# Kernel optimization log

Hardware: AMD Instinct MI355X
Metric: run time of the kernel (lower is better)

## Reference

```python
import jax, jax.numpy as jnp
import numpy as np

HIDDEN = 2048
N_HEADS = 16
N_KV = 4
HEAD_DIM = 128
B, T = 2, 2048


def setup_inputs() -> dict:
    key = jax.random.key(0)
    k1, k2, k3, k4 = jax.random.split(key, 4)
    x = jax.random.normal(k1, (B, T, HIDDEN), dtype=jnp.float32)
    # linear weights stored [out, in] like torch; we apply x @ W.T
    w_q = jax.random.normal(k2, (N_HEADS * HEAD_DIM, HIDDEN), dtype=jnp.float32) * (HIDDEN ** -0.5)
    w_kv = jax.random.normal(k3, (2 * N_KV * HEAD_DIM, HIDDEN), dtype=jnp.float32) * (HIDDEN ** -0.5)
    w_o = jax.random.normal(k4, (HIDDEN, N_HEADS * HEAD_DIM), dtype=jnp.float32) * ((N_HEADS * HEAD_DIM) ** -0.5)
    return {"x": x, "w_q": w_q, "w_kv": w_kv, "w_o": w_o}


def reference(x, w_q, w_kv, w_o):
    b, t, _ = x.shape
    groups = N_HEADS // N_KV
    scale = HEAD_DIM ** -0.5

    q = (x @ w_q.T).reshape(b, t, N_HEADS, HEAD_DIM).transpose(0, 2, 1, 3)  # [B,H,T,D]
    kv = x @ w_kv.T
    k, v = jnp.split(kv, 2, axis=-1)
    k = k.reshape(b, t, N_KV, HEAD_DIM).transpose(0, 2, 1, 3)  # [B,KV,T,D]
    v = v.reshape(b, t, N_KV, HEAD_DIM).transpose(0, 2, 1, 3)
    # repeat_interleave over head dim -> [B,H,T,D]
    k = jnp.repeat(k, groups, axis=1)
    v = jnp.repeat(v, groups, axis=1)

    scores = jnp.einsum('bhqd,bhkd->bhqk', q, k) * scale  # [B,H,T,T]
    causal = jnp.triu(jnp.ones((t, t), dtype=bool), k=1)
    scores = jnp.where(causal, -jnp.inf, scores)
    weights = jax.nn.softmax(scores, axis=-1)
    out = jnp.einsum('bhqk,bhkd->bhqd', weights, v)  # [B,H,T,D]
    out = out.transpose(0, 2, 1, 3).reshape(b, t, N_HEADS * HEAD_DIM)
    return out @ w_o.T
```

## Files before the change

### kernel.cpp

```cpp
#include <hip/hip_runtime.h>

typedef short bf16x8 __attribute__((ext_vector_type(8)));
typedef float f32x4 __attribute__((ext_vector_type(4)));
typedef unsigned int u32x4 __attribute__((ext_vector_type(4)));

__device__ __forceinline__ unsigned short f2bf(float f) {
    unsigned int u = __float_as_uint(f);
    u = (u + 0x7fff + ((u >> 16) & 1)) >> 16;
    return (unsigned short)u;
}
__device__ __forceinline__ float bf2f(short s) {
    return __uint_as_float(((unsigned int)(unsigned short)s) << 16);
}

__device__ __forceinline__ void async16(const void* g, void* l) {
    __builtin_amdgcn_global_load_lds(
        (const __attribute__((address_space(1))) void*)g,
        (__attribute__((address_space(3))) void*)l,
        16 , 0 , 0 );
}

__global__ __launch_bounds__(256) void castall(const float* __restrict__ x,
                                               const float* __restrict__ wq,
                                               const float* __restrict__ wkv,
                                               const float* __restrict__ wo,
                                               unsigned short* __restrict__ xb,
                                               unsigned short* __restrict__ wqkvb,
                                               unsigned short* __restrict__ wob) {
    int i = blockIdx.x * blockDim.x + threadIdx.x;
    const float* src; unsigned short* dst; int j;
    if (i < 2097152)      { src = x;   dst = xb;    j = i; }
    else if (i < 3145728) { src = wq;  dst = wqkvb; j = i - 2097152; }
    else if (i < 3670016) { src = wkv; dst = wqkvb + (size_t)2048 * 2048; j = i - 3145728; }
    else                  { src = wo;  dst = wob;   j = i - 3670016; }
    float4 f = ((const float4*)src)[j];
    ushort4 u;
    u.x = f2bf(f.x); u.y = f2bf(f.y); u.z = f2bf(f.z); u.w = f2bf(f.w);
    ((ushort4*)dst)[j] = u;
}

template <int NREP, typename OutT>
__global__ __launch_bounds__(512, 2) void gemm8p(const unsigned short* __restrict__ A,
                                                 const unsigned short* __restrict__ B,
                                                 OutT* __restrict__ C,
                                                 unsigned short* __restrict__ VtOut,
                                                 int N, int K, int NT,
                                                 int ncut, float qscale) {
    constexpr int NCH = 4 + NREP;
    __shared__ __attribute__((aligned(16))) unsigned short LA[2][256 * 64];
    __shared__ __attribute__((aligned(16))) unsigned short LB[2][NREP * 64 * 64];

    const int tid  = threadIdx.x;
    const int lane = tid & 63;
    const int w    = tid >> 6;
    const int quad = lane >> 4;
    const int l16  = lane & 15;
    const int wm   = w >> 2;
    const int wn   = w & 3;
    const int m0   = blockIdx.x * 256;
    const int n0   = blockIdx.y * (NREP * 64);
    const int swz  = (l16 & 7) << 3;

    const int lr = lane >> 3;
    const int ls = lane & 7;
    const int ss = ls ^ lr;
    const unsigned short* aSrc = A + (size_t)(m0 + w * 8 + lr) * K + ss * 8;
    const unsigned short* bSrc = B + (size_t)(n0 + w * 8 + lr) * K + ss * 8;

    f32x4 acc[8][NREP] = {};

    auto stage1 = [&](int nb, int t, int si) {
        if (si >= NCH) return;
        if (si < NREP) {
            async16(bSrc + (size_t)si * 64 * K + t * 64, &LB[nb][(si * 64 + w * 8) * 64]);
        } else {
            int j = si - NREP;
            int c = (j == 0) ? 0 : (j == 1) ? 2 : (j == 2) ? 1 : 3;
            async16(aSrc + (size_t)c * 64 * K + t * 64, &LA[nb][(c * 64 + w * 8) * 64]);
        }
    };

    auto phase = [&](int cur, int q, bf16x8 (&bf)[NREP][2], int tn, bool last) {
        bf16x8 af[2][2];
        if (q == 0) {
#pragma unroll
            for (int n = 0; n < NREP; ++n)
#pragma unroll
                for (int kk = 0; kk < 2; ++kk)
                    bf[n][kk] = *(const bf16x8*)&LB[cur][(size_t)(wn * (NREP * 16) + n * 16 + l16) * 64
                                                         + ((kk * 32 + quad * 8) ^ swz)];
        }
#pragma unroll
        for (int mi = 0; mi < 2; ++mi)
#pragma unroll
            for (int kk = 0; kk < 2; ++kk)
                af[mi][kk] = *(const bf16x8*)&LA[cur][(size_t)(wm * 128 + (q * 2 + mi) * 16 + l16) * 64
                                                      + ((kk * 32 + quad * 8) ^ swz)];
        if (!last) { stage1(cur ^ 1, tn, 2 * q); stage1(cur ^ 1, tn, 2 * q + 1); }
        if (q == 1) {
            if (last) asm volatile("s_waitcnt vmcnt(0)" ::: "memory");
            else      asm volatile("s_waitcnt vmcnt(4)" ::: "memory");
        }
        if (q == 3 && !last) asm volatile("s_waitcnt vmcnt(2)" ::: "memory");
        __builtin_amdgcn_s_barrier();
        asm volatile("s_waitcnt lgkmcnt(0)" ::: "memory");
        __builtin_amdgcn_sched_barrier(0);
        __builtin_amdgcn_s_setprio(1);
#pragma unroll
        for (int mi = 0; mi < 2; ++mi)
#pragma unroll
            for (int n = 0; n < NREP; ++n)
#pragma unroll
                for (int kk = 0; kk < 2; ++kk)
                    acc[q * 2 + mi][n] = __builtin_amdgcn_mfma_f32_16x16x32_bf16(
                        af[mi][kk], bf[n][kk], acc[q * 2 + mi][n], 0, 0, 0);
        __builtin_amdgcn_s_setprio(0);
        __builtin_amdgcn_s_barrier();
    };

    auto ktile = [&](int cur, int tn, bool last) {
        bf16x8 bf[NREP][2];
        phase(cur, 0, bf, tn, last);
        phase(cur, 1, bf, tn, last);
        phase(cur, 2, bf, tn, last);
        phase(cur, 3, bf, tn, last);
    };

#pragma unroll
    for (int s = 0; s < NCH; ++s) stage1(0, 0, s);
    asm volatile("s_waitcnt vmcnt(2)" ::: "memory");
    __builtin_amdgcn_s_barrier();

    int cur = 0;
    for (int t = 0; t < NT - 1; ++t) {
        ktile(cur, t + 1, false);
        cur ^= 1;
    }
    ktile(cur, 0, true);

#pragma unroll
    for (int m = 0; m < 8; ++m) {
        int row = m0 + wm * 128 + m * 16 + quad * 4;
#pragma unroll
        for (int n = 0; n < NREP; ++n) {
            int col = n0 + wn * (NREP * 16) + n * 16 + l16;
            f32x4 v = acc[m][n];
            float s = (col < ncut) ? qscale : 1.0f;
            if (VtOut != nullptr && col >= 2560) {
                int bb = row >> 11, t0 = row & 2047;
                ushort4 o;
                o.x = f2bf(v[0]); o.y = f2bf(v[1]); o.z = f2bf(v[2]); o.w = f2bf(v[3]);
                *(ushort4*)(VtOut + ((size_t)(bb * 512 + (col - 2560))) * 2048 + t0) = o;
            } else {
#pragma unroll
                for (int j = 0; j < 4; ++j) {
                    float vj = v[j] * s;
                    if constexpr (sizeof(OutT) == 4)
                        C[(size_t)(row + j) * N + col] = vj;
                    else
                        C[(size_t)(row + j) * N + col] = f2bf(vj);
                }
            }
        }
    }
}

__global__ __launch_bounds__(256, 2) void attn_fwd9(const unsigned short* __restrict__ QKV,
                                                    const unsigned short* __restrict__ Vt,
                                                    unsigned short* __restrict__ Opart,
                                                    float* __restrict__ lpart) {
    __shared__ __attribute__((aligned(16))) unsigned short Ks[64 * 128];
    __shared__ __attribute__((aligned(16))) unsigned short Vs[2][128 * 64];

    const int tid  = threadIdx.x;
    const int lane = tid & 63;
    const int w    = tid >> 6;
    const int quad = lane >> 4;
    const int l16  = lane & 15;
    const int swz  = (l16 & 7) << 3;

    const int hb   = blockIdx.x;
    const int h    = hb & 15;
    const int b    = hb >> 4;
    const int y    = blockIdx.y;
    const int p    = 15 - (y >> 1);
    const int half = y & 1;
    const int kvh  = h >> 2;
    const float M_FIX = 12.0f;

    const int ntot   = p + 1;
    const int tstart = half ? ntot : 0;
    const int tend   = half ? 2 * ntot : ntot;

    const int qbase = p * 128;
    const int qw0   = qbase + w * 32;
    const int qw1   = qw0 + 16;

    bf16x8 qf[2][4];
#pragma unroll
    for (int g = 0; g < 2; ++g)
#pragma unroll
        for (int kd = 0; kd < 4; ++kd)
            qf[g][kd] = *(const bf16x8*)(QKV + (size_t)(b * 2048 + qw0 + g * 16 + l16) * 3072
                                         + h * 128 + kd * 32 + quad * 8);

    f32x4 oacc[2][8] = {};
    f32x4 rs4[2] = {};

    const unsigned short* gk[4];
    const unsigned short* gv[4];
#pragma unroll
    for (int pp = 0; pp < 4; ++pp) {
        int r  = (4 * w + pp) * 4 + (lane >> 4);
        int s  = lane & 15;
        int sp = (s & 8) | ((s ^ r) & 7);
        gk[pp] = QKV + (size_t)(b * 2048 + r) * 3072 + 2048 + kvh * 128 + sp * 8;
        int d  = (4 * w + pp) * 8 + (lane >> 3);
        int sv = (lane & 7) ^ (d & 7);
        gv[pp] = Vt + ((size_t)(b * 4 + kvh) * 128 + d) * 2048 + sv * 8;
    }

    auto stageK = [&](int t) {
        const size_t ko = (size_t)t * 64;
#pragma unroll
        for (int pp = 0; pp < 4; ++pp)
            async16(gk[pp] + ko * 3072, &Ks[(4 * w + pp) * 512]);
    };
    auto stageV = [&](int nb, int t) {
        const size_t ko = (size_t)t * 64;
#pragma unroll
        for (int pp = 0; pp < 4; ++pp)
            async16(gv[pp] + ko, &Vs[nb][(4 * w + pp) * 512]);
    };

    stageK(tstart);
    stageV(0, tstart);
    int cur = 0;

    for (int t = tstart; t < tend; ++t) {
        __syncthreads();
        if (t + 1 < tend) stageV(cur ^ 1, t + 1);
        const int k0 = t * 64;
        const bool liveW = (k0 <= qw0 + 15);
        const bool live1 = (k0 <= qw1 + 15);

        bf16x8 pa[2][2];
        if (liveW) {
            f32x4 sacc[2][4] = {};
            __builtin_amdgcn_s_setprio(1);
#pragma unroll
            for (int kt = 0; kt < 4; ++kt) {
                bf16x8 kf[4];
#pragma unroll
                for (int kd = 0; kd < 4; ++kd)
                    kf[kd] = *(const bf16x8*)&Ks[(kt * 16 + l16) * 128
                                                 + ((kd * 32 + quad * 8) ^ swz)];
#pragma unroll
                for (int kd = 0; kd < 4; ++kd)
                    sacc[0][kt] = __builtin_amdgcn_mfma_f32_16x16x32_bf16(kf[kd], qf[0][kd], sacc[0][kt], 0, 0, 0);
                if (live1) {
#pragma unroll
                    for (int kd = 0; kd < 4; ++kd)
                        sacc[1][kt] = __builtin_amdgcn_mfma_f32_16x16x32_bf16(kf[kd], qf[1][kd], sacc[1][kt], 0, 0, 0);
                }
            }
            __builtin_amdgcn_s_setprio(0);

#pragma unroll
            for (int g = 0; g < 2; ++g) {
                if (g == 1 && !live1) continue;
                const int qwg  = qw0 + g * 16;
                const bool diag = (k0 + 63 > qwg);
                const int qrow = qwg + l16;
                unsigned int pk[4][2];
#pragma unroll
                for (int kt = 0; kt < 4; ++kt) {
                    float pvv[4];
#pragma unroll
                    for (int j = 0; j < 4; ++j) {
                        float pv = __expf(sacc[g][kt][j] - M_FIX);
                        if (diag) {
                            int key = k0 + kt * 16 + quad * 4 + j;
                            if (key > qrow) pv = 0.f;
                        }
                        rs4[g][j] += pv;
                        pvv[j] = pv;
                    }
                    asm("v_cvt_pk_bf16_f32 %0, %1, %2" : "=v"(pk[kt][0]) : "v"(pvv[0]), "v"(pvv[1]));
                    asm("v_cvt_pk_bf16_f32 %0, %1, %2" : "=v"(pk[kt][1]) : "v"(pvv[2]), "v"(pvv[3]));
                }
#pragma unroll
                for (int ks = 0; ks < 2; ++ks) {
                    unsigned int d0 = pk[2 * ks][0], s0 = pk[2 * ks + 1][0];
                    unsigned int d1 = pk[2 * ks][1], s1 = pk[2 * ks + 1][1];
                    asm("v_permlane32_swap_b32 %0, %1" : "+v"(d0), "+v"(s0));
                    asm("v_permlane16_swap_b32 %0, %1" : "+v"(d0), "+v"(s0));
                    asm("v_permlane32_swap_b32 %0, %1" : "+v"(d1), "+v"(s1));
                    asm("v_permlane16_swap_b32 %0, %1" : "+v"(d1), "+v"(s1));
                    u32x4 tt;
                    tt.x = d0;
                    tt.y = d1;
                    tt.z = s0;
                    tt.w = s1;
                    pa[g][ks] = __builtin_bit_cast(bf16x8, tt);
                }
            }
        }

        asm volatile("s_waitcnt lgkmcnt(0)" ::: "memory");
        __builtin_amdgcn_s_barrier();
        if (t + 1 < tend) stageK(t + 1);

        if (liveW) {
            __builtin_amdgcn_s_setprio(1);
#pragma unroll
            for (int dt = 0; dt < 8; ++dt) {
                bf16x8 vf[2];
#pragma unroll
                for (int ks = 0; ks < 2; ++ks)
                    vf[ks] = *(const bf16x8*)&Vs[cur][(dt * 16 + l16) * 64
                                                      + ((ks * 32 + quad * 8) ^ swz)];
#pragma unroll
                for (int ks = 0; ks < 2; ++ks)
                    oacc[0][dt] = __builtin_amdgcn_mfma_f32_16x16x32_bf16(pa[0][ks], vf[ks], oacc[0][dt], 0, 0, 0);
                if (live1) {
#pragma unroll
                    for (int ks = 0; ks < 2; ++ks)
                        oacc[1][dt] = __builtin_amdgcn_mfma_f32_16x16x32_bf16(pa[1][ks], vf[ks], oacc[1][dt], 0, 0, 0);
                }
            }
            __builtin_amdgcn_s_setprio(0);
        }
        cur ^= 1;
    }

#pragma unroll
    for (int g = 0; g < 2; ++g) {
        float r = (rs4[g][0] + rs4[g][1]) + (rs4[g][2] + rs4[g][3]);
        r += __shfl_xor(r, 16, 64);
        r += __shfl_xor(r, 32, 64);
        if (lane < 16)
            lpart[((size_t)(half * 2 + b) * 16 + h) * 2048 + qw0 + g * 16 + lane] = r;
#pragma unroll
        for (int dt = 0; dt < 8; ++dt)
#pragma unroll
            for (int j = 0; j < 4; ++j) {
                int qrow = qw0 + g * 16 + quad * 4 + j;
                Opart[(size_t)(half * 4096 + b * 2048 + qrow) * 2048 + h * 128 + dt * 16 + l16] =
                    f2bf(oacc[g][dt][j]);
            }
    }
}

__global__ __launch_bounds__(256) void combine(const unsigned short* __restrict__ Opart,
                                               const float* __restrict__ lpart,
                                               unsigned short* __restrict__ O) {
    const int r   = blockIdx.x;
    const int b   = r >> 11, row = r & 2047;
    const int col = threadIdx.x * 8;
    const int h   = col >> 7;
    bf16x8 a = *(const bf16x8*)(Opart + (size_t)r * 2048 + col);
    bf16x8 c = *(const bf16x8*)(Opart + (size_t)(4096 + r) * 2048 + col);
    float la = lpart[((size_t)(0 * 2 + b) * 16 + h) * 2048 + row];
    float lb = lpart[((size_t)(1 * 2 + b) * 16 + h) * 2048 + row];
    float inv = 1.0f / (la + lb);
    bf16x8 o;
#pragma unroll
    for (int i = 0; i < 8; ++i)
        o[i] = (short)f2bf((bf2f(a[i]) + bf2f(c[i])) * inv);
    *(bf16x8*)(O + (size_t)r * 2048 + col) = o;
}

extern "C" void kernel_launch(void* const* d_in, const int* in_sizes, int n_in,
                              void* d_out, int out_size, void* d_ws, size_t ws_size,
                              hipStream_t stream) {
    const float* x   = (const float*)d_in[0];
    const float* wq  = (const float*)d_in[1];
    const float* wkv = (const float*)d_in[2];
    const float* wo  = (const float*)d_in[3];
    float* out = (float*)d_out;

    char* ws = (char*)d_ws;
    size_t off = 0;
    auto alloc = [&](size_t bytes) { size_t o = off; off += (bytes + 255) & ~(size_t)255; return o; };
    unsigned short* xb    = (unsigned short*)(ws + alloc((size_t)4096 * 2048 * 2));
    unsigned short* wqkvb = (unsigned short*)(ws + alloc((size_t)3072 * 2048 * 2));
    unsigned short* wob   = (unsigned short*)(ws + alloc((size_t)2048 * 2048 * 2));
    unsigned short* QKVb  = (unsigned short*)(ws + alloc((size_t)4096 * 3072 * 2));
    unsigned short* Ab    = (unsigned short*)(ws + alloc((size_t)4096 * 2048 * 2));
    unsigned short* Vtb   = (unsigned short*)(ws + alloc((size_t)2 * 4 * 128 * 2048 * 2));
    unsigned short* Opart = (unsigned short*)(ws + alloc((size_t)2 * 4096 * 2048 * 2));
    float*          lpart = (float*)(ws + alloc((size_t)2 * 2 * 16 * 2048 * 4));

    const float qscale = 0.08838834764831845f;

    castall<<<18432, 256, 0, stream>>>(x, wq, wkv, wo, xb, wqkvb, wob);

    gemm8p<3, unsigned short><<<dim3(16, 16), 512, 0, stream>>>(xb, wqkvb, QKVb, Vtb,
                                                                3072, 2048, 32, 2048, qscale);

    attn_fwd9<<<dim3(32, 32), 256, 0, stream>>>(QKVb, Vtb, Opart, lpart);
    combine<<<4096, 256, 0, stream>>>(Opart, lpart, Ab);

    gemm8p<2, float><<<dim3(16, 16), 512, 0, stream>>>(Ab, wob, out, nullptr,
                                                       2048, 2048, 32, 0, 1.0f);
}
```

Baseline: 275.0 us.

## Restructure GEMM K-loop into two-phase pipeline with 4x2 warp layout

```diff
diff --git a/kernel.cpp b/kernel.cpp
--- a/kernel.cpp
+++ b/kernel.cpp
@@ -40,13 +40,15 @@
 }
 
 template <int NREP, typename OutT>
-__global__ __launch_bounds__(512, 2) void gemm8p(const unsigned short* __restrict__ A,
+__global__ __launch_bounds__(512, 2) void gemm2p(const unsigned short* __restrict__ A,
                                                  const unsigned short* __restrict__ B,
                                                  OutT* __restrict__ C,
                                                  unsigned short* __restrict__ VtOut,
                                                  int N, int K, int NT,
                                                  int ncut, float qscale) {
     constexpr int NCH = 4 + NREP;
+    constexpr int S0  = NCH - 3;
+    constexpr int NJ  = 2 * NREP;
     __shared__ __attribute__((aligned(16))) unsigned short LA[2][256 * 64];
     __shared__ __attribute__((aligned(16))) unsigned short LB[2][NREP * 64 * 64];
 
@@ -55,8 +57,8 @@
     const int w    = tid >> 6;
     const int quad = lane >> 4;
     const int l16  = lane & 15;
-    const int wm   = w >> 2;
-    const int wn   = w & 3;
+    const int wm   = w >> 1;
+    const int wn   = w & 1;
     const int m0   = blockIdx.x * 256;
     const int n0   = blockIdx.y * (NREP * 64);
     const int swz  = (l16 & 7) << 3;
@@ -67,84 +69,92 @@
     const unsigned short* aSrc = A + (size_t)(m0 + w * 8 + lr) * K + ss * 8;
     const unsigned short* bSrc = B + (size_t)(n0 + w * 8 + lr) * K + ss * 8;
 
-    f32x4 acc[8][NREP] = {};
+    f32x4 acc[4][NJ] = {};
 
     auto stage1 = [&](int nb, int t, int si) {
-        if (si >= NCH) return;
         if (si < NREP) {
             async16(bSrc + (size_t)si * 64 * K + t * 64, &LB[nb][(si * 64 + w * 8) * 64]);
         } else {
-            int j = si - NREP;
-            int c = (j == 0) ? 0 : (j == 1) ? 2 : (j == 2) ? 1 : 3;
+            int c = si - NREP;
             async16(aSrc + (size_t)c * 64 * K + t * 64, &LA[nb][(c * 64 + w * 8) * 64]);
         }
     };
 
-    auto phase = [&](int cur, int q, bf16x8 (&bf)[NREP][2], int tn, bool last) {
+#pragma unroll
+    for (int s = 0; s < NCH; ++s) stage1(0, 0, s);
+
+    for (int t = 0; t < NT; ++t) {
+        const int cur  = t & 1;
+        const bool more = (t + 1 < NT);
+
+        if (more) {
+#pragma unroll
+            for (int s = 0; s < S0; ++s) stage1(cur ^ 1, t + 1, s);
+            asm volatile("s_waitcnt vmcnt(%0)" :: "i"(S0) : "memory");
+        } else {
+            asm volatile("s_waitcnt vmcnt(0)" ::: "memory");
+        }
+        __builtin_amdgcn_s_barrier();
+
+        bf16x8 bf[NJ][2];
+#pragma unroll
+        for (int n = 0; n < NJ; ++n)
+#pragma unroll
+            for (int kk = 0; kk < 2; ++kk)
+                bf[n][kk] = *(const bf16x8*)&LB[cur][(size_t)(wn * (NJ * 16) + n * 16 + l16) * 64
+                                                     + ((kk * 32 + quad * 8) ^ swz)];
         bf16x8 af[2][2];
-        if (q == 0) {
-#pragma unroll
-            for (int n = 0; n < NREP; ++n)
-#pragma unroll
-                for (int kk = 0; kk < 2; ++kk)
-                    bf[n][kk] = *(const bf16x8*)&LB[cur][(size_t)(wn * (NREP * 16) + n * 16 + l16) * 64
-                                                         + ((kk * 32 + quad * 8) ^ swz)];
-        }
 #pragma unroll
         for (int mi = 0; mi < 2; ++mi)
 #pragma unroll
             for (int kk = 0; kk < 2; ++kk)
-                af[mi][kk] = *(const bf16x8*)&LA[cur][(size_t)(wm * 128 + (q * 2 + mi) * 16 + l16) * 64
+                af[mi][kk] = *(const bf16x8*)&LA[cur][(size_t)(wm * 64 + mi * 16 + l16) * 64
                                                       + ((kk * 32 + quad * 8) ^ swz)];
-        if (!last) { stage1(cur ^ 1, tn, 2 * q); stage1(cur ^ 1, tn, 2 * q + 1); }
-        if (q == 1) {
-            if (last) asm volatile("s_waitcnt vmcnt(0)" ::: "memory");
-            else      asm volatile("s_waitcnt vmcnt(4)" ::: "memory");
-        }
-        if (q == 3 && !last) asm volatile("s_waitcnt vmcnt(2)" ::: "memory");
-        __builtin_amdgcn_s_barrier();
         asm volatile("s_waitcnt lgkmcnt(0)" ::: "memory");
         __builtin_amdgcn_sched_barrier(0);
         __builtin_amdgcn_s_setprio(1);
 #pragma unroll
         for (int mi = 0; mi < 2; ++mi)
 #pragma unroll
-            for (int n = 0; n < NREP; ++n)
+            for (int n = 0; n < NJ; ++n)
 #pragma unroll
                 for (int kk = 0; kk < 2; ++kk)
-                    acc[q * 2 + mi][n] = __builtin_amdgcn_mfma_f32_16x16x32_bf16(
-                        af[mi][kk], bf[n][kk], acc[q * 2 + mi][n], 0, 0, 0);
+                    acc[mi][n] = __builtin_amdgcn_mfma_f32_16x16x32_bf16(
+                        af[mi][kk], bf[n][kk], acc[mi][n], 0, 0, 0);
+        __builtin_amdgcn_s_setprio(0);
+
+        if (more) {
+#pragma unroll
+            for (int s = S0; s < NCH; ++s) stage1(cur ^ 1, t + 1, s);
+        }
+#pragma unroll
+        for (int mi = 0; mi < 2; ++mi)
+#pragma unroll
+            for (int kk = 0; kk < 2; ++kk)
+                af[mi][kk] = *(const bf16x8*)&LA[cur][(size_t)(wm * 64 + 32 + mi * 16 + l16) * 64
+                                                      + ((kk * 32 + quad * 8) ^ swz)];
+        asm volatile("s_waitcnt lgkmcnt(0)" ::: "memory");
+        __builtin_amdgcn_sched_barrier(0);
+        __builtin_amdgcn_s_setprio(1);
+#pragma unroll
+        for (int mi = 0; mi < 2; ++mi)
+#pragma unroll
+            for (int n = 0; n < NJ; ++n)
+#pragma unroll
+                for (int kk = 0; kk < 2; ++kk)
+                    acc[2 + mi][n] = __builtin_amdgcn_mfma_f32_16x16x32_bf16(
+                        af[mi][kk], bf[n][kk], acc[2 + mi][n], 0, 0, 0);
         __builtin_amdgcn_s_setprio(0);
         __builtin_amdgcn_s_barrier();
-    };
-
-    auto ktile = [&](int cur, int tn, bool last) {
-        bf16x8 bf[NREP][2];
-        phase(cur, 0, bf, tn, last);
-        phase(cur, 1, bf, tn, last);
-        phase(cur, 2, bf, tn, last);
-        phase(cur, 3, bf, tn, last);
-    };
-
-#pragma unroll
-    for (int s = 0; s < NCH; ++s) stage1(0, 0, s);
-    asm volatile("s_waitcnt vmcnt(2)" ::: "memory");
-    __builtin_amdgcn_s_barrier();
-
-    int cur = 0;
-    for (int t = 0; t < NT - 1; ++t) {
-        ktile(cur, t + 1, false);
-        cur ^= 1;
     }
-    ktile(cur, 0, true);
-
-#pragma unroll
-    for (int m = 0; m < 8; ++m) {
-        int row = m0 + wm * 128 + m * 16 + quad * 4;
-#pragma unroll
-        for (int n = 0; n < NREP; ++n) {
-            int col = n0 + wn * (NREP * 16) + n * 16 + l16;
-            f32x4 v = acc[m][n];
+
+#pragma unroll
+    for (int am = 0; am < 4; ++am) {
+        int row = m0 + wm * 64 + am * 16 + quad * 4;
+#pragma unroll
+        for (int n = 0; n < NJ; ++n) {
+            int col = n0 + wn * (NJ * 16) + n * 16 + l16;
+            f32x4 v = acc[am][n];
             float s = (col < ncut) ? qscale : 1.0f;
             if (VtOut != nullptr && col >= 2560) {
                 int bb = row >> 11, t0 = row & 2047;
@@ -396,12 +406,12 @@
 
     castall<<<18432, 256, 0, stream>>>(x, wq, wkv, wo, xb, wqkvb, wob);
 
-    gemm8p<3, unsigned short><<<dim3(16, 16), 512, 0, stream>>>(xb, wqkvb, QKVb, Vtb,
+    gemm2p<3, unsigned short><<<dim3(16, 16), 512, 0, stream>>>(xb, wqkvb, QKVb, Vtb,
                                                                 3072, 2048, 32, 2048, qscale);
 
     attn_fwd9<<<dim3(32, 32), 256, 0, stream>>>(QKVb, Vtb, Opart, lpart);
     combine<<<4096, 256, 0, stream>>>(Opart, lpart, Ab);
 
-    gemm8p<2, float><<<dim3(16, 16), 512, 0, stream>>>(Ab, wob, out, nullptr,
+    gemm2p<2, float><<<dim3(16, 16), 512, 0, stream>>>(Ab, wob, out, nullptr,
                                                        2048, 2048, 32, 0, 1.0f);
 }
```

Result: slower. 289.5 us (+5.3%).
